# Optimization experiments

Hardware: AMD Instinct MI355X
Metric: run time of the kernel (lower is better)

## Reference

```python
import jax, jax.numpy as jnp
import numpy as np

Q_NUM = 2_000_000
V_NUM = 100_000
T_NUM = 200_000
T_CURVE = 20_000
N_DISC = 400_000
F = 8      # FEATURE_DIM
H = 64     # MLP hidden
OUT = 3    # OUT_DIM
UR = 0.002 # feature init range, as in the torch module


def setup_inputs() -> dict:
    key = jax.random.key(0)
    ks = jax.random.split(key, 18)
    Q = jax.random.uniform(ks[0], (Q_NUM, 2), dtype=jnp.float32)
    V = jax.random.uniform(ks[1], (V_NUM, 2), dtype=jnp.float32)
    T = jax.random.randint(ks[2], (T_NUM, 3), 0, V_NUM, dtype=jnp.int32)
    QT_idx = jax.random.randint(ks[3], (Q_NUM,), 0, T_NUM, dtype=jnp.int32)
    uv = jax.random.uniform(ks[4], (Q_NUM, 2), dtype=jnp.float32)
    s = uv.sum(-1, keepdims=True)
    QT_uv = jnp.where(s > 1.0, 1.0 - uv[:, ::-1], uv)  # valid barycentric: u+v<=1
    V_is_continuous = jax.random.bernoulli(ks[5], 0.7, (V_NUM,))
    T_adj = jax.random.randint(ks[6], (T_NUM, 6), 0, N_DISC, dtype=jnp.int32)
    inv = jax.random.bernoulli(ks[7], 0.2, (T_NUM, 6))
    T_adj_disc_feat_idx = jnp.where(inv, jnp.int32(-1), T_adj)
    T_inside_cubic_sign = jax.random.bernoulli(ks[8], 0.5, (T_CURVE,))
    seco = jax.random.randint(ks[9], (T_CURVE, 2), 0, N_DISC, dtype=jnp.int32)
    seco_T_adj_disc_feat_idx = jnp.where(jax.random.bernoulli(ks[10], 0.3, (T_CURVE, 2)), jnp.int32(-1), seco)
    uni = lambda k, shape: jax.random.uniform(k, shape, minval=-UR, maxval=UR, dtype=jnp.float32)
    V_continuous_feat = uni(ks[11], (V_NUM, F))
    V_discontinuous_feat = uni(ks[12], (N_DISC, F))
    V_curved_feat = uni(ks[13], (T_CURVE, F))
    def lin(k, i, o):
        lim = 1.0 / np.sqrt(i)
        return jax.random.uniform(k, (i, o), minval=-lim, maxval=lim, dtype=jnp.float32)
    w1 = lin(ks[14], F, H); b1 = jnp.zeros((H,), jnp.float32)
    w2 = lin(ks[15], H, H); b2 = jnp.zeros((H,), jnp.float32)
    w3 = lin(ks[16], H, OUT); b3 = jnp.zeros((OUT,), jnp.float32)
    return {
        'Q': Q, 'V': V, 'QT_uv': QT_uv,
        'V_continuous_feat': V_continuous_feat,
        'V_discontinuous_feat': V_discontinuous_feat,
        'V_curved_feat': V_curved_feat,
        'w1': w1, 'b1': b1, 'w2': w2, 'b2': b2, 'w3': w3, 'b3': b3,
        'T': T, 'QT_idx': QT_idx, 'V_is_continuous': V_is_continuous,
        'T_adj_disc_feat_idx': T_adj_disc_feat_idx,
        'T_inside_cubic_sign': T_inside_cubic_sign,
        'seco_T_adj_disc_feat_idx': seco_T_adj_disc_feat_idx,
        'T_NUM_CURVE': T_CURVE,
    }


def interpolate(QT_uv, V_continuous_feat, V_discontinuous_feat, V_curved_feat,
                T, QT_idx, V_is_continuous, T_adj_disc_feat_idx,
                T_inside_cubic_sign, seco_T_adj_disc_feat_idx, T_NUM_CURVE):
    u = QT_uv[:, 0]; v = QT_uv[:, 1]; w0 = 1.0 - u - v
    weights = jnp.stack([w0, u, v], axis=-1)                 # [Q,3]
    tv = T[QT_idx]                                           # [Q,3] vertex ids
    cont = V_continuous_feat[tv]                             # [Q,3,F]
    # primary per-corner discontinuous-feature index (stride-2 in flat T*6 layout)
    disc_idx = T_adj_disc_feat_idx[QT_idx][:, ::2]           # [Q,3]
    is_curved = QT_idx < T_NUM_CURVE                         # [Q]
    cid = jnp.clip(QT_idx, 0, T_NUM_CURVE - 1)               # safe curved id
    # curved triangles override corners 1,2 with secondary radial-feature links
    seco_q = seco_T_adj_disc_feat_idx[cid]                   # [Q,2]
    override = is_curved[:, None] & (seco_q >= 0)
    disc_idx = jnp.concatenate(
        [disc_idx[:, :1], jnp.where(override, seco_q, disc_idx[:, 1:])], axis=1)
    disc = V_discontinuous_feat[jnp.maximum(disc_idx, 0)]    # [Q,3,F]
    use_disc = (~V_is_continuous[tv]) & (disc_idx >= 0)      # [Q,3]
    corner_feat = jnp.where(use_disc[..., None], disc, cont) # [Q,3,F]
    interp = jnp.einsum('qc,qcf->qf', weights, corner_feat)  # [Q,F]
    # cubic-bubble curved contribution, signed by inside-cubic orientation
    sign = jnp.where(T_inside_cubic_sign[cid], 1.0, -1.0)
    bubble = 27.0 * w0 * u * v                               # 1 at centroid
    curved = (is_curved.astype(interp.dtype) * sign * bubble)[:, None] * V_curved_feat[cid]
    return interp + curved


def reference(Q, V, QT_uv, V_continuous_feat, V_discontinuous_feat, V_curved_feat,
              w1, b1, w2, b2, w3, b3,
              T, QT_idx, V_is_continuous, T_adj_disc_feat_idx,
              T_inside_cubic_sign, seco_T_adj_disc_feat_idx, T_NUM_CURVE):
    feat = interpolate(QT_uv, V_continuous_feat, V_discontinuous_feat, V_curved_feat,
                       T, QT_idx, V_is_continuous, T_adj_disc_feat_idx,
                       T_inside_cubic_sign, seco_T_adj_disc_feat_idx, T_NUM_CURVE)
    h = jax.nn.relu(feat @ w1 + b1)
    h = jax.nn.relu(h @ w2 + b2)
    return h @ w3 + b3
```

## Files before the change

kernel.cpp:

```cpp
#include <hip/hip_runtime.h>
#include <hip/hip_bf16.h>
#include <stdint.h>

#define Q_NUM   2000000
#define T_NUM   200000
#define T_CURVE 20000
#define NF      8
#define NH      64
#define NOUT    3

#define WS_REC_OFF   32768
#define WS_NEEDED    (WS_REC_OFF + (size_t)T_NUM * 128)

#define NWSF_W  5120
#define NWSF    5376

typedef float f32x16 __attribute__((ext_vector_type(16)));
typedef short s16x8  __attribute__((ext_vector_type(8)));

union FragU { int4 v; s16x8 s; unsigned u[4]; };

__device__ __forceinline__ unsigned short f2bf(float f) {
    __hip_bfloat16 h = __float2bfloat16(f);
    unsigned short u; __builtin_memcpy(&u, &h, 2); return u;
}
__device__ __forceinline__ float bf2f(unsigned short u) {
    unsigned v = ((unsigned)u) << 16; float f; __builtin_memcpy(&f, &v, 4); return f;
}

__global__ void prep_w(const float* __restrict__ w1, const float* __restrict__ b1,
                       const float* __restrict__ w2, const float* __restrict__ b2,
                       const float* __restrict__ w3, unsigned* __restrict__ wsf) {
    const int l = threadIdx.x;
    if (l >= 64) return;
    const int hb = l >> 5;
    for (int plane = 0; plane < 2; ++plane)
      for (int kb = 0; kb < 4; ++kb)
        for (int mb = 0; mb < 2; ++mb)
          for (int i = 0; i < 4; ++i) {
              const int j  = 32 * mb + (l & 31);
              const int k0 = 16 * kb + 8 * hb + 2 * i;
              const float v0 = w2[k0 * NH + j];
              const float v1 = w2[(k0 + 1) * NH + j];
              unsigned d;
              if (plane == 0) {
                  d = (unsigned)f2bf(v0) | ((unsigned)f2bf(v1) << 16);
              } else {
                  const float r0 = v0 - bf2f(f2bf(v0));
                  const float r1 = v1 - bf2f(f2bf(v1));
                  d = (unsigned)f2bf(r0) | ((unsigned)f2bf(r1) << 16);
              }
              wsf[(((plane * 4 + kb) * 2 + mb) * 64 + l) * 4 + i] = d;
          }
    for (int plane = 0; plane < 2; ++plane)
      for (int mb = 0; mb < 2; ++mb)
        for (int i = 0; i < 4; ++i) {
            const int j = 32 * mb + (l & 31);
            unsigned d = 0;
            if (hb == 0) {
                const int k0 = 2 * i;
                const float v0 = w1[k0 * NH + j];
                const float v1 = w1[(k0 + 1) * NH + j];
                if (plane == 0) {
                    d = (unsigned)f2bf(v0) | ((unsigned)f2bf(v1) << 16);
                } else {
                    const float r0 = v0 - bf2f(f2bf(v0));
                    const float r1 = v1 - bf2f(f2bf(v1));
                    d = (unsigned)f2bf(r0) | ((unsigned)f2bf(r1) << 16);
                }
            } else if (i == 0) {
                const float bv = b1[j];
                if (plane == 0) {
                    d = (unsigned)f2bf(bv);
                } else {
                    d = (unsigned)f2bf(bv - bf2f(f2bf(bv)));
                }
            }
            wsf[NWSF_W - 1024 + ((plane * 2 + mb) * 64 + l) * 4 + i] = d;
        }
    float4* ep = (float4*)&wsf[NWSF_W];
    ep[l] = make_float4(b2[l], w3[l * 3 + 0], w3[l * 3 + 1], w3[l * 3 + 2]);
}

__global__ __launch_bounds__(256) void build_rec(
    const float* __restrict__ Vcont,
    const float* __restrict__ Vdisc,
    const float* __restrict__ Vcurv,
    const int*   __restrict__ T,
    const void*  __restrict__ VisCont,
    const int*   __restrict__ Tadj,
    const void*  __restrict__ Tsign,
    const int*   __restrict__ seco,
    float4* __restrict__ rec)
{
    const uint32_t* probe = (const uint32_t*)VisCont;
    uint32_t m = 0;
#pragma unroll
    for (int i = 0; i < 16; ++i) m |= probe[i];
    const bool bool_is_byte = (m > 1u);

    const int t = blockIdx.x * blockDim.x + threadIdx.x;
    if (t >= T_NUM) return;

    const int tv0 = T[t * 3 + 0];
    const int tv1 = T[t * 3 + 1];
    const int tv2 = T[t * 3 + 2];

    int d0 = Tadj[t * 6 + 0];
    int d1 = Tadj[t * 6 + 2];
    int d2 = Tadj[t * 6 + 4];

    const bool is_curved = (t < T_CURVE);
    if (is_curved) {
        const int s0 = seco[t * 2 + 0];
        const int s1 = seco[t * 2 + 1];
        if (s0 >= 0) d1 = s0;
        if (s1 >= 0) d2 = s1;
    }

    auto rdbool = [&](const void* p, int idx) -> bool {
        return bool_is_byte ? (((const uint8_t*)p)[idx] != 0)
                            : (((const int*)p)[idx] != 0);
    };

    const bool use0 = (!rdbool(VisCont, tv0)) && (d0 >= 0);
    const bool use1 = (!rdbool(VisCont, tv1)) && (d1 >= 0);
    const bool use2 = (!rdbool(VisCont, tv2)) && (d2 >= 0);

    const float4* c0p = (const float4*)(use0 ? &Vdisc[(size_t)d0 * NF] : &Vcont[(size_t)tv0 * NF]);
    const float4* c1p = (const float4*)(use1 ? &Vdisc[(size_t)d1 * NF] : &Vcont[(size_t)tv1 * NF]);
    const float4* c2p = (const float4*)(use2 ? &Vdisc[(size_t)d2 * NF] : &Vcont[(size_t)tv2 * NF]);

    float4* rp = &rec[(size_t)t * 8];
    rp[0] = c0p[0]; rp[1] = c0p[1];
    rp[2] = c1p[0]; rp[3] = c1p[1];
    rp[4] = c2p[0]; rp[5] = c2p[1];

    float4 cv0 = make_float4(0.f, 0.f, 0.f, 0.f);
    float4 cv1 = cv0;
    if (is_curved) {
        const float s = rdbool(Tsign, t) ? 1.0f : -1.0f;
        const float4* cvp = (const float4*)&Vcurv[(size_t)t * NF];
        float4 a = cvp[0], b = cvp[1];
        cv0 = make_float4(s * a.x, s * a.y, s * a.z, s * a.w);
        cv1 = make_float4(s * b.x, s * b.y, s * b.z, s * b.w);
    }
    rp[6] = cv0; rp[7] = cv1;
}

__device__ __forceinline__ void mlp_block(const unsigned src[4], bool hb, int lane,
                                          const unsigned* slds, const float4* epb,
                                          float& p0, float& p1, float& p2)
{
    FragU fb;
    fb.u[0] = hb ? 0x00003F80u : src[0];
    fb.u[1] = hb ? 0u : src[1];
    fb.u[2] = hb ? 0u : src[2];
    fb.u[3] = hb ? 0u : src[3];

    unsigned pk[8][2];
#pragma unroll
    for (int mb = 0; mb < 2; ++mb) {
        FragU a1hi, a1lo;
        a1hi.v = *(const int4*)&slds[NWSF_W - 1024 + ((0 * 2 + mb) * 64 + lane) * 4];
        a1lo.v = *(const int4*)&slds[NWSF_W - 1024 + ((1 * 2 + mb) * 64 + lane) * 4];
        f32x16 accA;
#pragma unroll
        for (int z = 0; z < 16; ++z) accA[z] = 0.f;
        accA = __builtin_amdgcn_mfma_f32_32x32x16_bf16(a1hi.s, fb.s, accA, 0, 0, 0);
        accA = __builtin_amdgcn_mfma_f32_32x32x16_bf16(a1lo.s, fb.s, accA, 0, 0, 0);
#pragma unroll
        for (int hh = 0; hh < 4; ++hh) {
            const int rb = 4 * hh;
            const float v0 = fmaxf(accA[rb + 0], 0.f);
            const float v1 = fmaxf(accA[rb + 1], 0.f);
            const float v2 = fmaxf(accA[rb + 2], 0.f);
            const float v3 = fmaxf(accA[rb + 3], 0.f);
            pk[4 * mb + hh][0] = (unsigned)f2bf(v0) | ((unsigned)f2bf(v1) << 16);
            pk[4 * mb + hh][1] = (unsigned)f2bf(v2) | ((unsigned)f2bf(v3) << 16);
        }
    }

    FragU fr[4];
#pragma unroll
    for (int kb = 0; kb < 4; ++kb) {
        const unsigned own0 = hb ? pk[2 * kb + 1][0] : pk[2 * kb][0];
        const unsigned own1 = hb ? pk[2 * kb + 1][1] : pk[2 * kb][1];
        const unsigned X0   = hb ? pk[2 * kb][0] : pk[2 * kb + 1][0];
        const unsigned X1   = hb ? pk[2 * kb][1] : pk[2 * kb + 1][1];
        const unsigned Y0   = (unsigned)__shfl_xor((int)X0, 32);
        const unsigned Y1   = (unsigned)__shfl_xor((int)X1, 32);
        fr[kb].u[0] = hb ? Y0 : own0;
        fr[kb].u[1] = hb ? Y1 : own1;
        fr[kb].u[2] = hb ? own0 : Y0;
        fr[kb].u[3] = hb ? own1 : Y1;
    }

#pragma unroll
    for (int mb = 0; mb < 2; ++mb) {
        f32x16 acc;
#pragma unroll
        for (int z = 0; z < 16; ++z) acc[z] = 0.f;
#pragma unroll
        for (int kb = 0; kb < 4; ++kb) {
            FragU ahi, alo;
            ahi.v = *(const int4*)&slds[(((0 * 4 + kb) * 2 + mb) * 64 + lane) * 4];
            alo.v = *(const int4*)&slds[(((1 * 4 + kb) * 2 + mb) * 64 + lane) * 4];
            acc = __builtin_amdgcn_mfma_f32_32x32x16_bf16(ahi.s, fr[kb].s, acc, 0, 0, 0);
            acc = __builtin_amdgcn_mfma_f32_32x32x16_bf16(alo.s, fr[kb].s, acc, 0, 0, 0);
        }
#pragma unroll
        for (int r = 0; r < 16; ++r) {
            const int jr = (r & 3) + 8 * (r >> 2) + 32 * mb;
            const float4 e = epb[jr];
            const float tv = fmaxf(acc[r] + e.x, 0.f);
            p0 = fmaf(tv, e.y, p0);
            p1 = fmaf(tv, e.z, p1);
            p2 = fmaf(tv, e.w, p2);
        }
    }
}

template <bool REC>
__global__ __launch_bounds__(256) void dann_fwd_t(
    const float* __restrict__ QT_uv,
    const float* __restrict__ Vcont,
    const float* __restrict__ Vdisc,
    const float* __restrict__ Vcurv,
    const float* __restrict__ b3,
    const int*   __restrict__ T,
    const int*   __restrict__ QT_idx,
    const void*  __restrict__ VisCont,
    const int*   __restrict__ Tadj,
    const void*  __restrict__ Tsign,
    const int*   __restrict__ seco,
    const unsigned* __restrict__ wsf,
    const float4* __restrict__ rec,
    float* __restrict__ out)
{
    __shared__ unsigned slds[NWSF];
    for (int i = threadIdx.x; i < NWSF; i += 256) slds[i] = wsf[i];

    const int q  = blockIdx.x * blockDim.x + threadIdx.x;
    const int qc = (q < Q_NUM) ? q : (Q_NUM - 1);
    const int  lane    = threadIdx.x & 63;
    const bool hb      = (lane >= 32);
    const bool lo_half = !hb;

    const float2 uv = ((const float2*)QT_uv)[qc];
    const float u  = uv.x;
    const float v  = uv.y;
    const float w0 = 1.0f - u - v;
    const int   t  = QT_idx[qc];
    const float bub = 27.0f * w0 * u * v;

    float4 c0a, c0b, c1a, c1b, c2a, c2b, cva, cvb;
    float cf;

    if (REC) {
        const float4* rp = &rec[(size_t)t * 8];
        c0a = rp[0]; c0b = rp[1];
        c1a = rp[2]; c1b = rp[3];
        c2a = rp[4]; c2b = rp[5];
        cva = rp[6]; cvb = rp[7];
        cf = bub;
    } else {
        const uint32_t* probe = (const uint32_t*)VisCont;
        uint32_t m = 0;
#pragma unroll
        for (int i = 0; i < 16; ++i) m |= probe[i];
        const bool bool_is_byte = (m > 1u);

        const int tv0 = T[t * 3 + 0];
        const int tv1 = T[t * 3 + 1];
        const int tv2 = T[t * 3 + 2];
        int d0 = Tadj[t * 6 + 0];
        int d1 = Tadj[t * 6 + 2];
        int d2 = Tadj[t * 6 + 4];
        const bool is_curved = (t < T_CURVE);
        const int  cid = is_curved ? t : (T_CURVE - 1);
        const int  s0 = seco[cid * 2 + 0];
        const int  s1 = seco[cid * 2 + 1];
        if (is_curved && s0 >= 0) d1 = s0;
        if (is_curved && s1 >= 0) d2 = s1;
        auto rdbool = [&](const void* p, int i) -> bool {
            return bool_is_byte ? (((const uint8_t*)p)[i] != 0)
                                : (((const int*)p)[i] != 0);
        };
        const bool use0 = (!rdbool(VisCont, tv0)) && (d0 >= 0);
        const bool use1 = (!rdbool(VisCont, tv1)) && (d1 >= 0);
        const bool use2 = (!rdbool(VisCont, tv2)) && (d2 >= 0);
        const float4* c0p = (const float4*)(use0 ? &Vdisc[(size_t)d0 * NF] : &Vcont[(size_t)tv0 * NF]);
        const float4* c1p = (const float4*)(use1 ? &Vdisc[(size_t)d1 * NF] : &Vcont[(size_t)tv1 * NF]);
        const float4* c2p = (const float4*)(use2 ? &Vdisc[(size_t)d2 * NF] : &Vcont[(size_t)tv2 * NF]);
        c0a = c0p[0]; c0b = c0p[1];
        c1a = c1p[0]; c1b = c1p[1];
        c2a = c2p[0]; c2b = c2p[1];
        cf = 0.0f;
        if (is_curved) cf = rdbool(Tsign, cid) ? bub : -bub;
        const float4* cvp = (const float4*)&Vcurv[(size_t)cid * NF];
        cva = cvp[0]; cvb = cvp[1];
    }

    float feat[NF];
    {
        const float* a0 = (const float*)&c0a;  const float* bb0 = (const float*)&c0b;
        const float* a1 = (const float*)&c1a;  const float* bb1 = (const float*)&c1b;
        const float* a2 = (const float*)&c2a;  const float* bb2 = (const float*)&c2b;
        const float* av = (const float*)&cva;  const float* bv  = (const float*)&cvb;
#pragma unroll
        for (int f = 0; f < 4; ++f) {
            feat[f]     = w0 * a0[f]  + u * a1[f]  + v * a2[f]  + cf * av[f];
            feat[f + 4] = w0 * bb0[f] + u * bb1[f] + v * bb2[f] + cf * bv[f];
        }
    }

    unsigned pf[4];
#pragma unroll
    for (int i = 0; i < 4; ++i)
        pf[i] = (unsigned)f2bf(feat[2 * i]) | ((unsigned)f2bf(feat[2 * i + 1]) << 16);

    __syncthreads();

    const float4* epb = (const float4*)&slds[NWSF_W] + (hb ? 4 : 0);

    float pA0 = 0.f, pA1 = 0.f, pA2 = 0.f;
    mlp_block(pf, hb, lane, slds, epb, pA0, pA1, pA2);

    unsigned pfx[4];
#pragma unroll
    for (int i = 0; i < 4; ++i) pfx[i] = (unsigned)__shfl_xor((int)pf[i], 32);
    float pB0 = 0.f, pB1 = 0.f, pB2 = 0.f;
    mlp_block(pfx, hb, lane, slds, epb, pB0, pB1, pB2);

    const float sA0 = pA0 + __shfl_xor(pA0, 32);
    const float sA1 = pA1 + __shfl_xor(pA1, 32);
    const float sA2 = pA2 + __shfl_xor(pA2, 32);
    const float sB0 = pB0 + __shfl_xor(pB0, 32);
    const float sB1 = pB1 + __shfl_xor(pB1, 32);
    const float sB2 = pB2 + __shfl_xor(pB2, 32);

    const float o0 = (lo_half ? sA0 : sB0) + b3[0];
    const float o1 = (lo_half ? sA1 : sB1) + b3[1];
    const float o2 = (lo_half ? sA2 : sB2) + b3[2];

    if (q < Q_NUM) {
        const size_t off = (size_t)q * NOUT;
        out[off + 0] = o0;
        out[off + 1] = o1;
        out[off + 2] = o2;
    }
}

extern "C" void kernel_launch(void* const* d_in, const int* in_sizes, int n_in,
                              void* d_out, int out_size, void* d_ws, size_t ws_size,
                              hipStream_t stream) {
    const float* QT_uv  = (const float*)d_in[2];
    const float* Vcont  = (const float*)d_in[3];
    const float* Vdisc  = (const float*)d_in[4];
    const float* Vcurv  = (const float*)d_in[5];
    const float* w1     = (const float*)d_in[6];
    const float* b1     = (const float*)d_in[7];
    const float* w2     = (const float*)d_in[8];
    const float* b2     = (const float*)d_in[9];
    const float* w3     = (const float*)d_in[10];
    const float* b3     = (const float*)d_in[11];
    const int*   T      = (const int*)d_in[12];
    const int*   QT_idx = (const int*)d_in[13];
    const void*  VisC   = d_in[14];
    const int*   Tadj   = (const int*)d_in[15];
    const void*  Tsign  = d_in[16];
    const int*   seco   = (const int*)d_in[17];
    float* out = (float*)d_out;

    unsigned* wsf = (unsigned*)d_ws;
    prep_w<<<1, 64, 0, stream>>>(w1, b1, w2, b2, w3, wsf);

    const int block = 256;
    const int grid  = (Q_NUM + block - 1) / block;

    if (ws_size >= WS_NEEDED) {
        float4* rec = (float4*)((char*)d_ws + WS_REC_OFF);
        build_rec<<<(T_NUM + 255) / 256, 256, 0, stream>>>(Vcont, Vdisc, Vcurv,
                                                           T, VisC, Tadj, Tsign, seco, rec);
        dann_fwd_t<true><<<grid, block, 0, stream>>>(QT_uv, Vcont, Vdisc, Vcurv,
                                                     b3, T, QT_idx, VisC, Tadj, Tsign, seco,
                                                     wsf, rec, out);
    } else {
        dann_fwd_t<false><<<grid, block, 0, stream>>>(QT_uv, Vcont, Vdisc, Vcurv,
                                                      b3, T, QT_idx, VisC, Tadj, Tsign, seco,
                                                      wsf, (const float4*)nullptr, out);
    }
}
```

Before: 117.3 us.

## Split feature gather and MLP into separate kernels via bf16 workspace buffer

Adds a gather_feats kernel that interpolates per-query features from the per-triangle record and writes packed bf16 features to workspace. A separate dann_mlp kernel then reads those contiguous features and runs the MFMA MLP. The aim is to decouple the latency-bound random gather from the compute-heavy MLP, so each kernel gets its own occupancy and access pattern. The cost is an extra 32MB write and read and one more launch, and the path runs only when the workspace is large enough.

```diff
diff --git a/kernel.cpp b/kernel.cpp
--- a/kernel.cpp
+++ b/kernel.cpp
@@ -9,8 +9,10 @@
 #define NH      64
 #define NOUT    3
 
-#define WS_REC_OFF   32768
-#define WS_NEEDED    (WS_REC_OFF + (size_t)T_NUM * 128)
+#define WS_REC_OFF    32768
+#define WS_FEAT_OFF   25632768
+#define WS_NEED_REC   (WS_REC_OFF + (size_t)T_NUM * 128)
+#define WS_NEED_FEAT  (WS_FEAT_OFF + (size_t)Q_NUM * 16)
 
 #define NWSF_W  5120
 #define NWSF    5376
@@ -148,6 +150,48 @@
     rp[6] = cv0; rp[7] = cv1;
 }
 
+__global__ __launch_bounds__(256) void gather_feats(
+    const float* __restrict__ QT_uv,
+    const int*   __restrict__ QT_idx,
+    const float4* __restrict__ rec,
+    uint4* __restrict__ feats)
+{
+    for (int q = blockIdx.x * blockDim.x + threadIdx.x; q < Q_NUM;
+         q += gridDim.x * blockDim.x) {
+        const float2 uv = ((const float2*)QT_uv)[q];
+        const float u  = uv.x;
+        const float v  = uv.y;
+        const float w0 = 1.0f - u - v;
+        const int   t  = QT_idx[q];
+        const float cf = 27.0f * w0 * u * v;
+
+        const float4* rp = &rec[(size_t)t * 8];
+        const float4 c0a = rp[0], c0b = rp[1];
+        const float4 c1a = rp[2], c1b = rp[3];
+        const float4 c2a = rp[4], c2b = rp[5];
+        const float4 cva = rp[6], cvb = rp[7];
+
+        float feat[NF];
+        {
+            const float* a0 = (const float*)&c0a;  const float* bb0 = (const float*)&c0b;
+            const float* a1 = (const float*)&c1a;  const float* bb1 = (const float*)&c1b;
+            const float* a2 = (const float*)&c2a;  const float* bb2 = (const float*)&c2b;
+            const float* av = (const float*)&cva;  const float* bv  = (const float*)&cvb;
+#pragma unroll
+            for (int f = 0; f < 4; ++f) {
+                feat[f]     = w0 * a0[f]  + u * a1[f]  + v * a2[f]  + cf * av[f];
+                feat[f + 4] = w0 * bb0[f] + u * bb1[f] + v * bb2[f] + cf * bv[f];
+            }
+        }
+        uint4 pf;
+        pf.x = (unsigned)f2bf(feat[0]) | ((unsigned)f2bf(feat[1]) << 16);
+        pf.y = (unsigned)f2bf(feat[2]) | ((unsigned)f2bf(feat[3]) << 16);
+        pf.z = (unsigned)f2bf(feat[4]) | ((unsigned)f2bf(feat[5]) << 16);
+        pf.w = (unsigned)f2bf(feat[6]) | ((unsigned)f2bf(feat[7]) << 16);
+        feats[q] = pf;
+    }
+}
+
 __device__ __forceinline__ void mlp_block(const unsigned src[4], bool hb, int lane,
                                           const unsigned* slds, const float4* epb,
                                           float& p0, float& p1, float& p2)
@@ -221,8 +265,58 @@
     }
 }
 
+__global__ __launch_bounds__(256) void dann_mlp(
+    const uint4* __restrict__ feats,
+    const float* __restrict__ b3,
+    const unsigned* __restrict__ wsf,
+    float* __restrict__ out)
+{
+    __shared__ unsigned slds[NWSF];
+    for (int i = threadIdx.x; i < NWSF; i += 256) slds[i] = wsf[i];
+
+    const int q  = blockIdx.x * blockDim.x + threadIdx.x;
+    const int qc = (q < Q_NUM) ? q : (Q_NUM - 1);
+    const int  lane    = threadIdx.x & 63;
+    const bool hb      = (lane >= 32);
+    const bool lo_half = !hb;
+
+    const uint4 pfv = feats[qc];
+    unsigned pf[4] = { pfv.x, pfv.y, pfv.z, pfv.w };
+
+    __syncthreads();
+
+    const float4* epb = (const float4*)&slds[NWSF_W] + (hb ? 4 : 0);
+
+    float pA0 = 0.f, pA1 = 0.f, pA2 = 0.f;
+    mlp_block(pf, hb, lane, slds, epb, pA0, pA1, pA2);
+
+    unsigned pfx[4];
+#pragma unroll
+    for (int i = 0; i < 4; ++i) pfx[i] = (unsigned)__shfl_xor((int)pf[i], 32);
+    float pB0 = 0.f, pB1 = 0.f, pB2 = 0.f;
+    mlp_block(pfx, hb, lane, slds, epb, pB0, pB1, pB2);
+
+    const float sA0 = pA0 + __shfl_xor(pA0, 32);
+    const float sA1 = pA1 + __shfl_xor(pA1, 32);
+    const float sA2 = pA2 + __shfl_xor(pA2, 32);
+    const float sB0 = pB0 + __shfl_xor(pB0, 32);
+    const float sB1 = pB1 + __shfl_xor(pB1, 32);
+    const float sB2 = pB2 + __shfl_xor(pB2, 32);
+
+    const float o0 = (lo_half ? sA0 : sB0) + b3[0];
+    const float o1 = (lo_half ? sA1 : sB1) + b3[1];
+    const float o2 = (lo_half ? sA2 : sB2) + b3[2];
+
+    if (q < Q_NUM) {
+        const size_t off = (size_t)q * NOUT;
+        out[off + 0] = o0;
+        out[off + 1] = o1;
+        out[off + 2] = o2;
+    }
+}
+
 template <bool REC>
-__global__ __launch_bounds__(256) void dann_fwd_t(
+__global__ __launch_bounds__(256) void dann_fused(
     const float* __restrict__ QT_uv,
     const float* __restrict__ Vcont,
     const float* __restrict__ Vdisc,
@@ -379,15 +473,22 @@
     const int block = 256;
     const int grid  = (Q_NUM + block - 1) / block;
 
-    if (ws_size >= WS_NEEDED) {
+    if (ws_size >= WS_NEED_FEAT) {
+        float4* rec   = (float4*)((char*)d_ws + WS_REC_OFF);
+        uint4*  feats = (uint4*)((char*)d_ws + WS_FEAT_OFF);
+        build_rec<<<(T_NUM + 255) / 256, 256, 0, stream>>>(Vcont, Vdisc, Vcurv,
+                                                           T, VisC, Tadj, Tsign, seco, rec);
+        gather_feats<<<2048, 256, 0, stream>>>(QT_uv, QT_idx, rec, feats);
+        dann_mlp<<<grid, block, 0, stream>>>(feats, b3, wsf, out);
+    } else if (ws_size >= WS_NEED_REC) {
         float4* rec = (float4*)((char*)d_ws + WS_REC_OFF);
         build_rec<<<(T_NUM + 255) / 256, 256, 0, stream>>>(Vcont, Vdisc, Vcurv,
                                                            T, VisC, Tadj, Tsign, seco, rec);
-        dann_fwd_t<true><<<grid, block, 0, stream>>>(QT_uv, Vcont, Vdisc, Vcurv,
+        dann_fused<true><<<grid, block, 0, stream>>>(QT_uv, Vcont, Vdisc, Vcurv,
                                                      b3, T, QT_idx, VisC, Tadj, Tsign, seco,
                                                      wsf, rec, out);
     } else {
-        dann_fwd_t<false><<<grid, block, 0, stream>>>(QT_uv, Vcont, Vdisc, Vcurv,
+        dann_fused<false><<<grid, block, 0, stream>>>(QT_uv, Vcont, Vdisc, Vcurv,
                                                       b3, T, QT_idx, VisC, Tadj, Tsign, seco,
                                                       wsf, (const float4*)nullptr, out);
     }
```

Result: slower. 133.7 us (+13.9%).
